# Kernel tuning notes

Hardware: AMD Instinct MI355X
Metric: run time of the kernel (lower is better)

Reference implementation:

```python
import jax, jax.numpy as jnp
import numpy as np

ALPHA_LEAKY = 0.2
EPS = 1e-10


def setup_inputs() -> dict:
    key = jax.random.key(0)
    ks = jax.random.split(key, 7)
    Nq, Nk, E, D = 100000, 100000, 1600000, 64
    return {
        "query_nodes": jax.random.normal(ks[0], (Nq, D), dtype=jnp.float32),
        "key_value_nodes": jax.random.normal(ks[1], (Nk, D), dtype=jnp.float32),
        "edge_index": jax.random.randint(ks[2], (2, E), 0, Nq, dtype=jnp.int64),
        "proj_w": jax.random.normal(ks[3], (D, D), dtype=jnp.float32) * 0.1,
        "proj_b": jax.random.normal(ks[4], (D,), dtype=jnp.float32) * 0.1,
        "attend_w": jax.random.normal(ks[5], (1, 2 * D), dtype=jnp.float32) * 0.1,
        "attend_b": jax.random.normal(ks[6], (1,), dtype=jnp.float32) * 0.1,
    }


def reference(query_nodes, key_value_nodes, edge_index, proj_w, proj_b, attend_w, attend_b):
    Nq, D = query_nodes.shape
    qi, ki = edge_index[0], edge_index[1]  # [E], [E]
    # per-edge gathered + projected features (torch Linear: x @ W.T + b)
    query_proj = query_nodes[qi] @ proj_w.T + proj_b      # [E, D]
    kv_proj = key_value_nodes[ki] @ proj_w.T + proj_b     # [E, D]
    # attend(concat([qp, kp])) == qp @ Wq.T + kp @ Wk.T + b  (avoids [E,2D] concat)
    wq, wk = attend_w[:, :D], attend_w[:, D:]
    e = query_proj @ wq[0] + kv_proj @ wk[0] + attend_b[0]  # [E]
    e = jax.nn.leaky_relu(e, negative_slope=ALPHA_LEAKY)
    # segment-wise (per query node) numerically-stable softmax
    e_max = jax.ops.segment_max(e, qi, num_segments=Nq)    # [Nq] (-inf for empty)
    e_exp = jnp.exp(e - e_max[qi])                          # [E]
    e_sum = jax.ops.segment_sum(e_exp, qi, num_segments=Nq)  # [Nq]
    attention = e_exp / (e_sum[qi] + EPS)                   # [E]  (dropout = identity in eval)
    # weighted scatter-add aggregation back to query nodes
    weighted_values = kv_proj * attention[:, None]          # [E, D]
    aggregated_context = jax.ops.segment_sum(weighted_values, qi, num_segments=Nq)  # [Nq, D]
    return aggregated_context
```

## Files before the change

### kernel.cpp

```cpp
#include <hip/hip_runtime.h>

#define ALPHA_LEAKY 0.2f
#define EPS_F 1e-10f

#define BSHIFT 7
#define BRANGE 128
#define NBMAX 1024
#define CHUNK_F 4096
#define KBUF_CAP 3072

using half4_t = __attribute__((ext_vector_type(4))) _Float16;
using f32x4 = __attribute__((ext_vector_type(4))) float;

__device__ __forceinline__ unsigned short f2bf(float x) {
  unsigned int u = __float_as_uint(x);
  return (unsigned short)((u + 0x7fffu + ((u >> 16) & 1u)) >> 16);
}

__global__ __launch_bounds__(256, 2) void bin_proj_kernel(
    const int* __restrict__ eq, const int* __restrict__ ek,
    int* __restrict__ gcursor, int2* __restrict__ pairs, int E, int NB,
    int binBlocks,
    const float* __restrict__ qnodes, const float* __restrict__ kvnodes,
    const float* __restrict__ W, const float* __restrict__ pb,
    const float* __restrict__ aw, unsigned int* __restrict__ Kp16,
    float* __restrict__ sq, float* __restrict__ sk,
    int Nq, int Nk, int projBlocks) {
  const int t = threadIdx.x;

  if (blockIdx.x < binBlocks) {
    __shared__ int lcnt[NBMAX];
    __shared__ int lbase[NBMAX];
    for (int i = t; i < NBMAX; i += 256) lcnt[i] = 0;
    __syncthreads();

    const int cbase = blockIdx.x * CHUNK_F;
    int4 qv[4], kv[4];
#pragma unroll
    for (int j = 0; j < 4; ++j) {
      const int e0 = cbase + (((j << 8) + t) << 2);
      if (e0 + 3 < E) {
        qv[j] = *(const int4*)(eq + e0);
        kv[j] = *(const int4*)(ek + e0);
      } else {
        int tq[4] = {-1, -1, -1, -1}, tk[4] = {0, 0, 0, 0};
        for (int r = 0; r < 4; ++r)
          if (e0 + r < E) { tq[r] = eq[e0 + r]; tk[r] = ek[e0 + r]; }
        qv[j] = make_int4(tq[0], tq[1], tq[2], tq[3]);
        kv[j] = make_int4(tk[0], tk[1], tk[2], tk[3]);
      }
      if (qv[j].x >= 0) atomicAdd(&lcnt[qv[j].x >> BSHIFT], 1);
      if (qv[j].y >= 0) atomicAdd(&lcnt[qv[j].y >> BSHIFT], 1);
      if (qv[j].z >= 0) atomicAdd(&lcnt[qv[j].z >> BSHIFT], 1);
      if (qv[j].w >= 0) atomicAdd(&lcnt[qv[j].w >> BSHIFT], 1);
    }
    __syncthreads();
    for (int i = t; i < NB; i += 256) {
      lbase[i] = lcnt[i] ? atomicAdd(&gcursor[i], lcnt[i]) : 0;
      lcnt[i] = 0;
    }
    __syncthreads();
#pragma unroll
    for (int j = 0; j < 4; ++j) {
      const int qs[4] = {qv[j].x, qv[j].y, qv[j].z, qv[j].w};
      const int ks[4] = {kv[j].x, kv[j].y, kv[j].z, kv[j].w};
#pragma unroll
      for (int r = 0; r < 4; ++r) {
        if (qs[r] >= 0) {
          const int b = qs[r] >> BSHIFT;
          const int idx = lbase[b] + atomicAdd(&lcnt[b], 1);
          if (idx < KBUF_CAP)
            pairs[(size_t)b * KBUF_CAP + idx] = make_int2(qs[r], ks[r]);
        }
      }
    }
    return;
  }

  __shared__ float pt0[256];
  __shared__ __align__(16) float us[64];
  __shared__ float cq_s;
  const int lane = t & 63;
  const int waveId = (blockIdx.x - binBlocks) * 4 + (t >> 6);
  const int nWaves = projBlocks * 4;

  {
    const int pd = t & 63, og = t >> 6;
    float s0 = 0.f;
#pragma unroll
    for (int oo = 0; oo < 16; ++oo) {
      const int o = og * 16 + oo;
      s0 = fmaf(aw[o], W[o * 64 + pd], s0);
    }
    pt0[t] = s0;
  }
  __syncthreads();
  if (t < 64) {
    us[t] = (pt0[t] + pt0[t + 64]) + (pt0[t + 128] + pt0[t + 192]);
    if (t == 0) {
      float c0 = 0.f;
      for (int o = 0; o < 64; ++o) c0 = fmaf(aw[o], pb[o], c0);
      cq_s = c0;
    }
  }
  __syncthreads();

  {
    const int sub = lane & 15, ng = lane >> 4;
    const float4 uv = ((const float4*)us)[sub];
    const float c = cq_s;
    for (int base = waveId * 4; base < Nq; base += nWaves * 4) {
      const int n = base + ng;
      float s = 0.f;
      if (n < Nq) {
        const float4 x = *(const float4*)(qnodes + (size_t)n * 64 + sub * 4);
        s = x.x * uv.x + x.y * uv.y + x.z * uv.z + x.w * uv.w;
      }
#pragma unroll
      for (int off = 1; off <= 8; off <<= 1) s += __shfl_xor(s, off, 64);
      if (sub == 0 && n < Nq) sq[n] = s + c;
    }
  }

  const int c = lane & 15, g = lane >> 4;

  half4_t Bf[4][4];
  float pbv[4];
#pragma unroll
  for (int nt = 0; nt < 4; ++nt) {
    pbv[nt] = pb[nt * 16 + c];
#pragma unroll
    for (int ks = 0; ks < 4; ++ks) {
      const float4 wv =
          *(const float4*)(W + (size_t)(nt * 16 + c) * 64 + ks * 16 + g * 4);
      half4_t h;
      h[0] = (_Float16)wv.x;
      h[1] = (_Float16)wv.y;
      h[2] = (_Float16)wv.z;
      h[3] = (_Float16)wv.w;
      Bf[nt][ks] = h;
    }
  }
  const float a0 = aw[64 + c], a1 = aw[80 + c], a2 = aw[96 + c],
              a3 = aw[112 + c];

  const int ntiles = (Nk + 15) >> 4;
  for (int tile = waveId; tile < ntiles; tile += nWaves) {
    const int n0 = tile << 4;
    const int arow = n0 + c;
    const bool aok = arow < Nk;
    const float* xr = kvnodes + (size_t)arow * 64 + g * 4;

    half4_t Af[4];
#pragma unroll
    for (int ks = 0; ks < 4; ++ks) {
      const float4 xv =
          aok ? *(const float4*)(xr + ks * 16) : make_float4(0.f, 0.f, 0.f, 0.f);
      half4_t h;
      h[0] = (_Float16)xv.x;
      h[1] = (_Float16)xv.y;
      h[2] = (_Float16)xv.z;
      h[3] = (_Float16)xv.w;
      Af[ks] = h;
    }

    f32x4 acc0 = {pbv[0], pbv[0], pbv[0], pbv[0]};
    f32x4 acc1 = {pbv[1], pbv[1], pbv[1], pbv[1]};
    f32x4 acc2 = {pbv[2], pbv[2], pbv[2], pbv[2]};
    f32x4 acc3 = {pbv[3], pbv[3], pbv[3], pbv[3]};
#pragma unroll
    for (int ks = 0; ks < 4; ++ks) {
      acc0 = __builtin_amdgcn_mfma_f32_16x16x16f16(Af[ks], Bf[0][ks], acc0, 0, 0, 0);
      acc1 = __builtin_amdgcn_mfma_f32_16x16x16f16(Af[ks], Bf[1][ks], acc1, 0, 0, 0);
      acc2 = __builtin_amdgcn_mfma_f32_16x16x16f16(Af[ks], Bf[2][ks], acc2, 0, 0, 0);
      acc3 = __builtin_amdgcn_mfma_f32_16x16x16f16(Af[ks], Bf[3][ks], acc3, 0, 0, 0);
    }

#pragma unroll
    for (int r = 0; r < 4; ++r) {
      const int node = n0 + g * 4 + r;
      if (node < Nk) {
        const unsigned int u0 =
            ((unsigned int)f2bf(acc1[r]) << 16) | f2bf(acc0[r]);
        const unsigned int u1 =
            ((unsigned int)f2bf(acc3[r]) << 16) | f2bf(acc2[r]);
        unsigned int* kp = Kp16 + (size_t)node * 32;
        kp[c] = u0;
        kp[16 + c] = u1;
      }
    }

    float ws0 = acc0[0] * a0 + acc1[0] * a1 + acc2[0] * a2 + acc3[0] * a3;
    float ws1 = acc0[1] * a0 + acc1[1] * a1 + acc2[1] * a2 + acc3[1] * a3;
    float ws2 = acc0[2] * a0 + acc1[2] * a1 + acc2[2] * a2 + acc3[2] * a3;
    float ws3 = acc0[3] * a0 + acc1[3] * a1 + acc2[3] * a2 + acc3[3] * a3;
#pragma unroll
    for (int off = 1; off <= 8; off <<= 1) {
      ws0 += __shfl_xor(ws0, off, 64);
      ws1 += __shfl_xor(ws1, off, 64);
      ws2 += __shfl_xor(ws2, off, 64);
      ws3 += __shfl_xor(ws3, off, 64);
    }
    if (c == 0) {
      const int nb4 = n0 + g * 4;
      if (nb4 + 3 < Nk) {
        *(float4*)(sk + nb4) = make_float4(ws0, ws1, ws2, ws3);
      } else {
        if (nb4 + 0 < Nk) sk[nb4 + 0] = ws0;
        if (nb4 + 1 < Nk) sk[nb4 + 1] = ws1;
        if (nb4 + 2 < Nk) sk[nb4 + 2] = ws2;
        if (nb4 + 3 < Nk) sk[nb4 + 3] = ws3;
      }
    }
  }
}

__global__ __launch_bounds__(512, 6) void sort_agg_kernel(
    const int2* __restrict__ pairs, const int* __restrict__ gcursor,
    const float* __restrict__ sq, const float* __restrict__ sk,
    const float* __restrict__ ab, const unsigned int* __restrict__ Kp16,
    float* __restrict__ out, int Nq) {
  __shared__ int lcnt[BRANGE];
  __shared__ int lcur[BRANGE];
  __shared__ int lstart[BRANGE + 1];
  __shared__ int kibuf[KBUF_CAP];
  __shared__ int wso2[2];

  const int t = threadIdx.x;
  const int b = blockIdx.x;
  const int qlo = b << BSHIFT;
  int n = gcursor[b];
  if (n > KBUF_CAP) n = KBUF_CAP;
  const size_t base = (size_t)b * KBUF_CAP;

  if (t < BRANGE) lcnt[t] = 0;
  __syncthreads();

  int2 pv[6];
  int np = 0;
#pragma unroll
  for (int r = 0; r < 6; ++r) {
    const int i = t + (r << 9);
    if (i < n) { pv[r] = pairs[base + i]; ++np; }
  }
#pragma unroll
  for (int r = 0; r < 6; ++r)
    if (r < np) atomicAdd(&lcnt[pv[r].x - qlo], 1);
  __syncthreads();

  const int lane = t & 63, wv = t >> 6;
  int v = 0, x = 0;
  if (t < BRANGE) {
    v = lcnt[t];
    x = v;
#pragma unroll
    for (int off = 1; off < 64; off <<= 1) {
      const int y = __shfl_up(x, off, 64);
      if (lane >= off) x += y;
    }
    if (lane == 63) wso2[wv] = x;
  }
  __syncthreads();
  if (t < BRANGE) {
    const int excl = ((wv == 1) ? wso2[0] : 0) + x - v;
    lstart[t] = excl;
    lcur[t] = excl;
    if (t == BRANGE - 1) lstart[BRANGE] = excl + v;
  }
  __syncthreads();

#pragma unroll
  for (int r = 0; r < 6; ++r)
    if (r < np) kibuf[atomicAdd(&lcur[pv[r].x - qlo], 1)] = pv[r].y;
  __syncthreads();

  const int ng = lane >> 3, dg = lane & 7;
  const float abv = ab[0];
#pragma unroll
  for (int pass = 0; pass < 2; ++pass) {
    const int l = (pass << 6) + (wv << 3) + ng;
    const int node = qlo + l;
    const bool act = node < Nq;
    const int s = act ? lstart[l] : 0;
    const int e = act ? lstart[l + 1] : 0;
    const float sqn = act ? sq[node] + abv : 0.f;

    float acc[8] = {0.f, 0.f, 0.f, 0.f, 0.f, 0.f, 0.f, 0.f};
    float wsum = 0.f;
    const int jm = e - 1;
#pragma unroll 1
    for (int j = s; j < e; j += 4) {
      const int ka = kibuf[j];
      const int kb = kibuf[min(j + 1, jm)];
      const int kc = kibuf[min(j + 2, jm)];
      const int kd = kibuf[min(j + 3, jm)];
      const float ea = sk[ka];
      const float eb = sk[kb];
      const float ec = sk[kc];
      const float ed = sk[kd];
      const uint4 ua = *(const uint4*)(Kp16 + (size_t)ka * 32 + (dg << 2));
      const uint4 ub = *(const uint4*)(Kp16 + (size_t)kb * 32 + (dg << 2));
      const uint4 uc = *(const uint4*)(Kp16 + (size_t)kc * 32 + (dg << 2));
      const uint4 ud = *(const uint4*)(Kp16 + (size_t)kd * 32 + (dg << 2));

      float xa = sqn + ea; xa = xa > 0.f ? xa : ALPHA_LEAKY * xa;
      float xb = sqn + eb; xb = xb > 0.f ? xb : ALPHA_LEAKY * xb;
      float xc = sqn + ec; xc = xc > 0.f ? xc : ALPHA_LEAKY * xc;
      float xd = sqn + ed; xd = xd > 0.f ? xd : ALPHA_LEAKY * xd;
      const float wa = __expf(xa);
      const float wb = (j + 1 < e) ? __expf(xb) : 0.f;
      const float wc = (j + 2 < e) ? __expf(xc) : 0.f;
      const float wd = (j + 3 < e) ? __expf(xd) : 0.f;

#define ACC8(W, U)                                             \
  acc[0] = fmaf(W, __uint_as_float(U.x << 16), acc[0]);        \
  acc[1] = fmaf(W, __uint_as_float(U.x & 0xffff0000u), acc[1]);\
  acc[2] = fmaf(W, __uint_as_float(U.y << 16), acc[2]);        \
  acc[3] = fmaf(W, __uint_as_float(U.y & 0xffff0000u), acc[3]);\
  acc[4] = fmaf(W, __uint_as_float(U.z << 16), acc[4]);        \
  acc[5] = fmaf(W, __uint_as_float(U.z & 0xffff0000u), acc[5]);\
  acc[6] = fmaf(W, __uint_as_float(U.w << 16), acc[6]);        \
  acc[7] = fmaf(W, __uint_as_float(U.w & 0xffff0000u), acc[7]);
      ACC8(wa, ua)
      ACC8(wb, ub)
      ACC8(wc, uc)
      ACC8(wd, ud)
#undef ACC8
      wsum += (wa + wb) + (wc + wd);
    }

    if (act) {
      const float inv = 1.0f / (wsum + EPS_F);
      const int obase = ((dg & 3) << 2) + ((dg >> 2) << 5);
      float4 r0 = {acc[0] * inv, acc[2] * inv, acc[4] * inv, acc[6] * inv};
      float4 r1 = {acc[1] * inv, acc[3] * inv, acc[5] * inv, acc[7] * inv};
      float* o = out + (size_t)node * 64 + obase;
      *(float4*)o = r0;
      *(float4*)(o + 16) = r1;
    }
  }
}

extern "C" void kernel_launch(void* const* d_in, const int* in_sizes, int n_in,
                              void* d_out, int out_size, void* d_ws, size_t ws_size,
                              hipStream_t stream) {
  const float* qnodes = (const float*)d_in[0];
  const float* kvnodes = (const float*)d_in[1];
  const int* ei = (const int*)d_in[2];
  const float* W = (const float*)d_in[3];
  const float* pb = (const float*)d_in[4];
  const float* aw = (const float*)d_in[5];
  const float* ab = (const float*)d_in[6];

  const int Nq = in_sizes[0] / 64;
  const int Nk = in_sizes[1] / 64;
  const int E = in_sizes[2] / 2;
  const int NB = (Nq + BRANGE - 1) >> BSHIFT;

  const int* eq = ei;
  const int* ek = ei + E;

  char* ws = (char*)d_ws;
  int2* pairs = (int2*)ws;
  unsigned int* Kp16 =
      (unsigned int*)(pairs + (size_t)NBMAX * KBUF_CAP);
  float* sq = (float*)(Kp16 + (size_t)Nk * 32);
  float* sk = sq + Nq;
  int* gcursor = (int*)(sk + Nk);

  hipMemsetAsync(gcursor, 0, NBMAX * sizeof(int), stream);

  const int binBlocks = (E + CHUNK_F - 1) / CHUNK_F;
  const int projBlocks = 1664;
  bin_proj_kernel<<<binBlocks + projBlocks, 256, 0, stream>>>(
      eq, ek, gcursor, pairs, E, NB, binBlocks, qnodes, kvnodes, W, pb, aw,
      Kp16, sq, sk, Nq, Nk, projBlocks);

  sort_agg_kernel<<<NB, 512, 0, stream>>>(pairs, gcursor, sq, sk, ab, Kp16,
                                          (float*)d_out, Nq);
}
```

Measured before the change: 177.2 us.

## Pack edge pairs into 32-bit words and interleave bin and projection blocks

Edge pairs are now stored as one 32-bit word, a 7-bit local query offset combined with a 20-bit key index, instead of an int2. This halves the scatter-write and read traffic between the binning and aggregation kernels. Bin blocks are interleaved one in every five with projection blocks so the atomic-heavy binning work spreads across the GPU instead of running first. The projection block count now follows the edge count (four per bin block), and launch_bounds drops the min-blocks hint. The packing assumes Nk fits in 20 bits.

```diff
diff --git a/kernel.cpp b/kernel.cpp
--- a/kernel.cpp
+++ b/kernel.cpp
@@ -17,24 +17,26 @@
   return (unsigned short)((u + 0x7fffu + ((u >> 16) & 1u)) >> 16);
 }
 
-__global__ __launch_bounds__(256, 2) void bin_proj_kernel(
+__global__ __launch_bounds__(256) void bin_proj_kernel(
     const int* __restrict__ eq, const int* __restrict__ ek,
-    int* __restrict__ gcursor, int2* __restrict__ pairs, int E, int NB,
-    int binBlocks,
+    int* __restrict__ gcursor, unsigned int* __restrict__ pairs, int E,
+    int NB, int binBlocks,
     const float* __restrict__ qnodes, const float* __restrict__ kvnodes,
     const float* __restrict__ W, const float* __restrict__ pb,
     const float* __restrict__ aw, unsigned int* __restrict__ Kp16,
     float* __restrict__ sq, float* __restrict__ sk,
     int Nq, int Nk, int projBlocks) {
   const int t = threadIdx.x;
-
-  if (blockIdx.x < binBlocks) {
+  const bool isBin = (blockIdx.x % 5) == 0;
+
+  if (isBin) {
+    const int bb = blockIdx.x / 5;
     __shared__ int lcnt[NBMAX];
     __shared__ int lbase[NBMAX];
     for (int i = t; i < NBMAX; i += 256) lcnt[i] = 0;
     __syncthreads();
 
-    const int cbase = blockIdx.x * CHUNK_F;
+    const int cbase = bb * CHUNK_F;
     int4 qv[4], kv[4];
 #pragma unroll
     for (int j = 0; j < 4; ++j) {
@@ -70,7 +72,9 @@
           const int b = qs[r] >> BSHIFT;
           const int idx = lbase[b] + atomicAdd(&lcnt[b], 1);
           if (idx < KBUF_CAP)
-            pairs[(size_t)b * KBUF_CAP + idx] = make_int2(qs[r], ks[r]);
+            pairs[(size_t)b * KBUF_CAP + idx] =
+                ((unsigned int)(qs[r] & (BRANGE - 1)) << 20) |
+                (unsigned int)ks[r];
         }
       }
     }
@@ -81,7 +85,8 @@
   __shared__ __align__(16) float us[64];
   __shared__ float cq_s;
   const int lane = t & 63;
-  const int waveId = (blockIdx.x - binBlocks) * 4 + (t >> 6);
+  const int projId = blockIdx.x - blockIdx.x / 5 - 1;
+  const int waveId = projId * 4 + (t >> 6);
   const int nWaves = projBlocks * 4;
 
   {
@@ -216,7 +221,7 @@
 }
 
 __global__ __launch_bounds__(512, 6) void sort_agg_kernel(
-    const int2* __restrict__ pairs, const int* __restrict__ gcursor,
+    const unsigned int* __restrict__ pairs, const int* __restrict__ gcursor,
     const float* __restrict__ sq, const float* __restrict__ sk,
     const float* __restrict__ ab, const unsigned int* __restrict__ Kp16,
     float* __restrict__ out, int Nq) {
@@ -236,7 +241,7 @@
   if (t < BRANGE) lcnt[t] = 0;
   __syncthreads();
 
-  int2 pv[6];
+  unsigned int pv[6];
   int np = 0;
 #pragma unroll
   for (int r = 0; r < 6; ++r) {
@@ -245,7 +250,7 @@
   }
 #pragma unroll
   for (int r = 0; r < 6; ++r)
-    if (r < np) atomicAdd(&lcnt[pv[r].x - qlo], 1);
+    if (r < np) atomicAdd(&lcnt[pv[r] >> 20], 1);
   __syncthreads();
 
   const int lane = t & 63, wv = t >> 6;
@@ -271,7 +276,8 @@
 
 #pragma unroll
   for (int r = 0; r < 6; ++r)
-    if (r < np) kibuf[atomicAdd(&lcur[pv[r].x - qlo], 1)] = pv[r].y;
+    if (r < np)
+      kibuf[atomicAdd(&lcur[pv[r] >> 20], 1)] = (int)(pv[r] & 0xFFFFFu);
   __syncthreads();
 
   const int ng = lane >> 3, dg = lane & 7;
@@ -361,9 +367,8 @@
   const int* ek = ei + E;
 
   char* ws = (char*)d_ws;
-  int2* pairs = (int2*)ws;
-  unsigned int* Kp16 =
-      (unsigned int*)(pairs + (size_t)NBMAX * KBUF_CAP);
+  unsigned int* pairs = (unsigned int*)ws;
+  unsigned int* Kp16 = pairs + (size_t)NBMAX * KBUF_CAP;
   float* sq = (float*)(Kp16 + (size_t)Nk * 32);
   float* sk = sq + Nq;
   int* gcursor = (int*)(sk + Nk);
@@ -371,8 +376,8 @@
   hipMemsetAsync(gcursor, 0, NBMAX * sizeof(int), stream);
 
   const int binBlocks = (E + CHUNK_F - 1) / CHUNK_F;
-  const int projBlocks = 1664;
-  bin_proj_kernel<<<binBlocks + projBlocks, 256, 0, stream>>>(
+  const int projBlocks = binBlocks * 4;
+  bin_proj_kernel<<<binBlocks * 5, 256, 0, stream>>>(
       eq, ek, gcursor, pairs, E, NB, binBlocks, qnodes, kvnodes, W, pb, aw,
       Kp16, sq, sk, Nq, Nk, projBlocks);
 
```

New measurement: 178.2 us. No clear change (+0.6%).
